# Kernel optimization log

Measured on AMD Instinct MI355X. Metric: run time of the kernel, lower is better.

The kernel has to match this reference:

```python
import jax
import jax.numpy as jnp
from jax import lax
import numpy as np

B, T, C, L = 512, 512, 128, 80
BLANK = C - 1  # Keras ctc_batch_cost uses last class as blank
NEG = -1e30
EPS = 1e-7


def setup_inputs() -> dict:
    key = jax.random.key(0)
    k1, k2 = jax.random.split(key)
    # y_pred: positive "probability-like" activations, as ctc_batch_cost expects
    y_pred = jax.random.uniform(k1, (B, T, C), dtype=jnp.float32)
    # labels: non-blank symbols in [0, C-2]
    y_true = jax.random.randint(k2, (B, L), 0, C - 1, dtype=jnp.int64)
    return {"y_true": y_true, "y_pred": y_pred}


def _ctc_loss(log_probs, labels):
    """log_probs: [B,T,C] log-softmax; labels: [B,L] ints. Returns [B,1] loss."""
    b, t, c = log_probs.shape
    l = labels.shape[1]
    s = 2 * l + 1
    # extended label sequence: blank, l1, blank, l2, ..., blank  -> [B,S]
    ext = jnp.full((b, s), BLANK, dtype=labels.dtype).at[:, 1::2].set(labels)
    # per-time log-prob of each extended symbol: [B,T,S]
    lp = jnp.take_along_axis(log_probs, ext[:, None, :], axis=2)
    # skip-transition allowed where symbol is non-blank and differs from s-2
    ext_m2 = jnp.concatenate([jnp.full((b, 2), BLANK, ext.dtype), ext[:, :-2]], axis=1)
    allow2 = (ext != BLANK) & (ext != ext_m2)  # [B,S]

    alpha0 = (jnp.full((b, s), NEG, dtype=log_probs.dtype)
              .at[:, 0].set(lp[:, 0, 0])
              .at[:, 1].set(lp[:, 0, 1]))

    neg1 = jnp.full((b, 1), NEG, dtype=log_probs.dtype)
    neg2 = jnp.full((b, 2), NEG, dtype=log_probs.dtype)

    def step(alpha, lp_t):
        a1 = jnp.concatenate([neg1, alpha[:, :-1]], axis=1)
        a2 = jnp.concatenate([neg2, alpha[:, :-2]], axis=1)
        a2 = jnp.where(allow2, a2, NEG)
        m = jnp.maximum(jnp.maximum(alpha, a1), a2)
        lse = m + jnp.log(jnp.exp(alpha - m) + jnp.exp(a1 - m) + jnp.exp(a2 - m))
        return lp_t + lse, None

    lp_t_first = jnp.swapaxes(lp, 0, 1)  # [T,B,S]
    alphaT, _ = lax.scan(step, alpha0, lp_t_first[1:])
    loss = -jnp.logaddexp(alphaT[:, s - 1], alphaT[:, s - 2])  # [B]
    return loss[:, None]


def reference(y_true, y_pred):
    # K.ctc_batch_cost: log(y_pred + eps), then tf.nn.ctc_loss (softmax inside)
    log_probs = jax.nn.log_softmax(jnp.log(y_pred + EPS), axis=-1)
    return _ctc_loss(log_probs, y_true)
```

## Files before the change

kernel.cpp:

```cpp
#include <hip/hip_runtime.h>

#define B_ 512
#define T_ 512
#define C_ 128
#define L_ 80
#define BLANK_ 127
#define EPS_ 1e-7f
#define LN2_ 0.6931471805599453f

#define LOG2F(x) __builtin_amdgcn_logf(x)

template <int CTRL>
__device__ __forceinline__ int dpp_i(int x) {
  return __builtin_amdgcn_update_dpp(0, x, CTRL, 0xF, 0xF, true);
}
template <int CTRL>
__device__ __forceinline__ float dpp_f(float x) {
  return __int_as_float(
      __builtin_amdgcn_update_dpp(0, __float_as_int(x), CTRL, 0xF, 0xF, true));
}
#define DPP_WSHR1 0x138
#define DPP_XOR1  0xB1
#define DPP_XOR2  0x4E
#define DPP_HMIRR 0x141
#define DPP_MIRR  0x140

__global__ __launch_bounds__(256) void ctc_fused(
    const int* __restrict__ labels,
    const float* __restrict__ y_pred,
    float* __restrict__ out)
{
  const int b = blockIdx.x, tid = threadIdx.x;
  const int wid = tid >> 6, lane = tid & 63;
  const float* gp = y_pred + (size_t)b * T_ * C_;

  __shared__ float ring[4 * 1024];
  __shared__ float comb[4];

  const bool evenLane = ((lane & 1) == 0);

  int ea = BLANK_, eb = BLANK_;
  float m0 = 0.f, m1 = 0.f, m2 = 0.f;
  float A0 = 0.f, A1 = 0.f, A2 = 0.f;
  int E = 0;
  if (wid == 0) {
    auto labAt = [&](int k) -> int {
      return (k >= 0 && k < L_) ? labels[b * L_ + k] : BLANK_;
    };
    if (evenLane) {
      const int k1 = (3 * lane) >> 1;
      ea = labAt(k1); eb = ea;
      m1 = ((k1 < L_) && (k1 == 0 || ea != labAt(k1 - 1))) ? 1.f : 0.f;
    } else {
      const int k0 = (3 * lane - 1) >> 1;
      const int k2 = k0 + 1;
      ea = labAt(k0); eb = labAt(k2);
      m0 = ((k0 < L_) && (k0 == 0 || ea != labAt(k0 - 1))) ? 1.f : 0.f;
      m2 = ((k2 < L_) && (eb != ea)) ? 1.f : 0.f;
    }
    A0 = (lane == 0) ? 1.f : 0.f;
  }

  const int rgrp = lane >> 3, j16 = lane & 7;
  float4 SA[8];
  float Sacc = 0.f;

  auto loadpair = [&](int P) {
    #pragma unroll
    for (int h = 0; h < 2; ++h) {
      const float4* src =
          (const float4*)(gp + (size_t)(16 * P + 8 * h + rgrp) * C_) + 4 * j16;
      #pragma unroll
      for (int k = 0; k < 4; ++k) SA[4 * h + k] = src[k];
    }
  };
  auto preppair = [&](int P) {
    #pragma unroll
    for (int h = 0; h < 2; ++h) {
      const int blk = 2 * P + h;
      float4* wd = (float4*)(ring + (blk & 3) * 1024 + rgrp * C_ + 16 * j16);
      float s = 0.f;
      #pragma unroll
      for (int k = 0; k < 4; ++k) {
        float4 v = SA[4 * h + k];
        v.x += EPS_; v.y += EPS_; v.z += EPS_; v.w += EPS_;
        wd[k] = v;
        s += (v.x + v.y) + (v.z + v.w);
      }
      s += dpp_f<DPP_XOR1>(s);
      s += dpp_f<DPP_XOR2>(s);
      s += dpp_f<DPP_HMIRR>(s);
      Sacc += LOG2F(s);
    }
  };

  auto stepBlock = [&](const float* g, const float* h, const float* p) {
    const int EL = dpp_i<DPP_WSHR1>(E);
    const int d = E - EL;
    #pragma unroll
    for (int j = 0; j < 8; ++j) {
      const float p1 = dpp_f<DPP_WSHR1>(A1);
      const float p2 = dpp_f<DPP_WSHR1>(A2);
      const float p1p = ldexpf(p1, d);
      const float p2p = ldexpf(p2, d);
      const float q0 = evenLane ? p[j] : g[j];
      const float q1 = evenLane ? g[j] : p[j];
      const float q2 = evenLane ? p[j] : h[j];
      const float t0 = q0 * fmaf(m0, p1p, A0 + p2p);
      const float t1 = q1 * fmaf(m1, p2p, A1 + A0);
      const float t2 = q2 * fmaf(m2, A0, A2 + A1);
      A0 = t0; A1 = t1; A2 = t2;
    }
    const float mx = fmaxf(fmaxf(A0, A1), A2);
    int ee = (int)((__float_as_uint(mx) >> 23) & 255u) - 127;
    const bool z = (mx == 0.f);
    ee = z ? 0 : ee;
    A0 = ldexpf(A0, -ee); A1 = ldexpf(A1, -ee); A2 = ldexpf(A2, -ee);
    E = z ? EL : (E - ee);
  };

  if (wid != 0) {
    loadpair(wid - 1);
    if (wid == 1) { preppair(0); loadpair(3); }
  }
  __syncthreads();

  for (int k = 0; k < 32; ++k) {
    if (wid == 0) {
      const float* rb0 = ring + ((2 * k) & 3) * 1024;
      const float* rb1 = ring + ((2 * k + 1) & 3) * 1024;
      float gA[8], hA[8], pA[8], gB[8], hB[8], pB[8];
      #pragma unroll
      for (int j = 0; j < 8; ++j) {
        gA[j] = rb0[j * C_ + ea];
        hA[j] = rb0[j * C_ + eb];
        pA[j] = rb0[j * C_ + BLANK_];
      }
      #pragma unroll
      for (int j = 0; j < 8; ++j) {
        gB[j] = rb1[j * C_ + ea];
        hB[j] = rb1[j * C_ + eb];
        pB[j] = rb1[j * C_ + BLANK_];
      }
      stepBlock(gA, hA, pA);
      stepBlock(gB, hB, pB);
    } else {
      const int P = k + 1;
      if (P < 32 && (P % 3) == (wid - 1)) {
        preppair(P);
        if (P + 3 < 32) loadpair(P + 3);
      }
    }
    __syncthreads();
  }

  if (wid != 0) {
    float s = Sacc;
    s += dpp_f<DPP_XOR1>(s);
    s += dpp_f<DPP_XOR2>(s);
    s += dpp_f<DPP_HMIRR>(s);
    s += dpp_f<DPP_MIRR>(s);
    s += __shfl_xor(s, 16, 64);
    s += __shfl_xor(s, 32, 64);
    if (lane == 0) comb[wid] = s * 0.125f;
  }
  __syncthreads();

  if (wid == 0 && lane == 53) {
    const float Stot = comb[1] + comb[2] + comb[3];
    out[b] = LN2_ * (Stot - (LOG2F(A0 + A1) - (float)E));
  }
}

extern "C" void kernel_launch(void* const* d_in, const int* in_sizes, int n_in,
                              void* d_out, int out_size, void* d_ws, size_t ws_size,
                              hipStream_t stream) {
  const int*   labels = (const int*)d_in[0];
  const float* y_pred = (const float*)d_in[1];
  float*       out    = (float*)d_out;
  ctc_fused<<<dim3(B_), dim3(256), 0, stream>>>(labels, y_pred, out);
}
```

Before: 194.3 us.

## Decouple recursion wave from normalizer waves with direct global gathers

```diff
diff --git a/kernel.cpp b/kernel.cpp
--- a/kernel.cpp
+++ b/kernel.cpp
@@ -34,127 +34,123 @@
   const int wid = tid >> 6, lane = tid & 63;
   const float* gp = y_pred + (size_t)b * T_ * C_;
 
-  __shared__ float ring[4 * 1024];
   __shared__ float comb[4];
 
   const bool evenLane = ((lane & 1) == 0);
 
-  int ea = BLANK_, eb = BLANK_;
-  float m0 = 0.f, m1 = 0.f, m2 = 0.f;
   float A0 = 0.f, A1 = 0.f, A2 = 0.f;
   int E = 0;
+
   if (wid == 0) {
     auto labAt = [&](int k) -> int {
       return (k >= 0 && k < L_) ? labels[b * L_ + k] : BLANK_;
     };
+    int ea, eb;
+    float m0, m1, m2;
     if (evenLane) {
       const int k1 = (3 * lane) >> 1;
       ea = labAt(k1); eb = ea;
+      m0 = 0.f; m2 = 0.f;
       m1 = ((k1 < L_) && (k1 == 0 || ea != labAt(k1 - 1))) ? 1.f : 0.f;
     } else {
       const int k0 = (3 * lane - 1) >> 1;
       const int k2 = k0 + 1;
       ea = labAt(k0); eb = labAt(k2);
       m0 = ((k0 < L_) && (k0 == 0 || ea != labAt(k0 - 1))) ? 1.f : 0.f;
+      m1 = 0.f;
       m2 = ((k2 < L_) && (eb != ea)) ? 1.f : 0.f;
     }
     A0 = (lane == 0) ? 1.f : 0.f;
-  }
 
-  const int rgrp = lane >> 3, j16 = lane & 7;
-  float4 SA[8];
-  float Sacc = 0.f;
+    const float* pea = gp + ea;
+    const float* peb = gp + eb;
+    const float* pbl = gp + BLANK_;
 
-  auto loadpair = [&](int P) {
-    #pragma unroll
-    for (int h = 0; h < 2; ++h) {
+    float gaA[8], gbA[8], pbA[8];
+    float gaB[8], gbB[8], pbB[8];
+    float gaC[8], gbC[8], pbC[8];
+
+    auto loadG = [&](float (&g)[8], float (&h)[8], float (&p)[8], int t0) {
+      #pragma unroll
+      for (int j = 0; j < 8; ++j) {
+        g[j] = pea[(t0 + j) * C_];
+        h[j] = peb[(t0 + j) * C_];
+        p[j] = pbl[(t0 + j) * C_];
+      }
+    };
+    auto stepG = [&](float (&g)[8], float (&h)[8], float (&p)[8]) {
+      const int EL = dpp_i<DPP_WSHR1>(E);
+      const int d = E - EL;
+      #pragma unroll
+      for (int j = 0; j < 8; ++j) {
+        const float p1 = dpp_f<DPP_WSHR1>(A1);
+        const float p2 = dpp_f<DPP_WSHR1>(A2);
+        const float p1p = ldexpf(p1, d);
+        const float p2p = ldexpf(p2, d);
+        const float q0 = (evenLane ? p[j] : g[j]) + EPS_;
+        const float q1 = (evenLane ? g[j] : p[j]) + EPS_;
+        const float q2 = (evenLane ? p[j] : h[j]) + EPS_;
+        const float t0 = q0 * fmaf(m0, p1p, A0 + p2p);
+        const float t1 = q1 * fmaf(m1, p2p, A1 + A0);
+        const float t2 = q2 * fmaf(m2, A0, A2 + A1);
+        A0 = t0; A1 = t1; A2 = t2;
+      }
+      const float mx = fmaxf(fmaxf(A0, A1), A2);
+      int ee = (int)((__float_as_uint(mx) >> 23) & 255u) - 127;
+      const bool z = (mx == 0.f);
+      ee = z ? 0 : ee;
+      A0 = ldexpf(A0, -ee); A1 = ldexpf(A1, -ee); A2 = ldexpf(A2, -ee);
+      E = z ? EL : (E - ee);
+    };
+
+    loadG(gaA, gbA, pbA, 0);
+    loadG(gaB, gbB, pbB, 8);
+    for (int g = 0; g < 63; g += 3) {
+      loadG(gaC, gbC, pbC, 8 * (g + 2));
+      stepG(gaA, gbA, pbA);
+      loadG(gaA, gbA, pbA, 8 * (g + 3));
+      stepG(gaB, gbB, pbB);
+      if (g + 4 < 64) loadG(gaB, gbB, pbB, 8 * (g + 4));
+      stepG(gaC, gbC, pbC);
+    }
+    stepG(gaA, gbA, pbA);
+  } else {
+    const int w = wid - 1;
+    const int rgrp = lane >> 3, j16 = lane & 7;
+    const int N = (64 - w + 2) / 3;
+    float4 S0[4], S1[4], S2[4];
+    float Sacc = 0.f;
+
+    auto loadB = [&](float4 (&S)[4], int i) {
+      const int blk = w + 3 * i;
       const float4* src =
-          (const float4*)(gp + (size_t)(16 * P + 8 * h + rgrp) * C_) + 4 * j16;
+          (const float4*)(gp + (size_t)(8 * blk + rgrp) * C_) + 4 * j16;
       #pragma unroll
-      for (int k = 0; k < 4; ++k) SA[4 * h + k] = src[k];
-    }
-  };
-  auto preppair = [&](int P) {
-    #pragma unroll
-    for (int h = 0; h < 2; ++h) {
-      const int blk = 2 * P + h;
-      float4* wd = (float4*)(ring + (blk & 3) * 1024 + rgrp * C_ + 16 * j16);
+      for (int k = 0; k < 4; ++k) S[k] = src[k];
+    };
+    auto sumB = [&](float4 (&S)[4]) {
       float s = 0.f;
       #pragma unroll
       for (int k = 0; k < 4; ++k) {
-        float4 v = SA[4 * h + k];
+        float4 v = S[k];
         v.x += EPS_; v.y += EPS_; v.z += EPS_; v.w += EPS_;
-        wd[k] = v;
         s += (v.x + v.y) + (v.z + v.w);
       }
       s += dpp_f<DPP_XOR1>(s);
       s += dpp_f<DPP_XOR2>(s);
       s += dpp_f<DPP_HMIRR>(s);
       Sacc += LOG2F(s);
+    };
+
+    loadB(S0, 0);
+    if (1 < N) loadB(S1, 1);
+    if (2 < N) loadB(S2, 2);
+    for (int i = 0; i < N; i += 3) {
+      sumB(S0); if (i + 3 < N) loadB(S0, i + 3);
+      if (i + 1 < N) { sumB(S1); if (i + 4 < N) loadB(S1, i + 4); }
+      if (i + 2 < N) { sumB(S2); if (i + 5 < N) loadB(S2, i + 5); }
     }
-  };
 
-  auto stepBlock = [&](const float* g, const float* h, const float* p) {
-    const int EL = dpp_i<DPP_WSHR1>(E);
-    const int d = E - EL;
-    #pragma unroll
-    for (int j = 0; j < 8; ++j) {
-      const float p1 = dpp_f<DPP_WSHR1>(A1);
-      const float p2 = dpp_f<DPP_WSHR1>(A2);
-      const float p1p = ldexpf(p1, d);
-      const float p2p = ldexpf(p2, d);
-      const float q0 = evenLane ? p[j] : g[j];
-      const float q1 = evenLane ? g[j] : p[j];
-      const float q2 = evenLane ? p[j] : h[j];
-      const float t0 = q0 * fmaf(m0, p1p, A0 + p2p);
-      const float t1 = q1 * fmaf(m1, p2p, A1 + A0);
-      const float t2 = q2 * fmaf(m2, A0, A2 + A1);
-      A0 = t0; A1 = t1; A2 = t2;
-    }
-    const float mx = fmaxf(fmaxf(A0, A1), A2);
-    int ee = (int)((__float_as_uint(mx) >> 23) & 255u) - 127;
-    const bool z = (mx == 0.f);
-    ee = z ? 0 : ee;
-    A0 = ldexpf(A0, -ee); A1 = ldexpf(A1, -ee); A2 = ldexpf(A2, -ee);
-    E = z ? EL : (E - ee);
-  };
-
-  if (wid != 0) {
-    loadpair(wid - 1);
-    if (wid == 1) { preppair(0); loadpair(3); }
-  }
-  __syncthreads();
-
-  for (int k = 0; k < 32; ++k) {
-    if (wid == 0) {
-      const float* rb0 = ring + ((2 * k) & 3) * 1024;
-      const float* rb1 = ring + ((2 * k + 1) & 3) * 1024;
-      float gA[8], hA[8], pA[8], gB[8], hB[8], pB[8];
-      #pragma unroll
-      for (int j = 0; j < 8; ++j) {
-        gA[j] = rb0[j * C_ + ea];
-        hA[j] = rb0[j * C_ + eb];
-        pA[j] = rb0[j * C_ + BLANK_];
-      }
-      #pragma unroll
-      for (int j = 0; j < 8; ++j) {
-        gB[j] = rb1[j * C_ + ea];
-        hB[j] = rb1[j * C_ + eb];
-        pB[j] = rb1[j * C_ + BLANK_];
-      }
-      stepBlock(gA, hA, pA);
-      stepBlock(gB, hB, pB);
-    } else {
-      const int P = k + 1;
-      if (P < 32 && (P % 3) == (wid - 1)) {
-        preppair(P);
-        if (P + 3 < 32) loadpair(P + 3);
-      }
-    }
-    __syncthreads();
-  }
-
-  if (wid != 0) {
     float s = Sacc;
     s += dpp_f<DPP_XOR1>(s);
     s += dpp_f<DPP_XOR2>(s);
@@ -164,6 +160,7 @@
     s += __shfl_xor(s, 32, 64);
     if (lane == 0) comb[wid] = s * 0.125f;
   }
+
   __syncthreads();
 
   if (wid == 0 && lane == 53) {
```

New measurement: 212.3 us. 9.3% more time.
